# Optimization experiments

Hardware: AMD Instinct MI355X
Metric: run time of the kernel (lower is better)

## Reference

```python
import jax, jax.numpy as jnp
import numpy as np

N = 4096          # vocab / support size (Nini == Nfin)
NBB = 64          # number of topics (columns of b)
NUM_ITER_MAX = 30
STOP_THR = 1e-9


def setup_inputs() -> dict:
    key = jax.random.key(0)
    k1, k2, k3, k4 = jax.random.split(key, 4)
    a = jax.random.uniform(k1, (N, 1), dtype=jnp.float32)
    a = a / jnp.sum(a)                       # source distribution
    b = jax.random.uniform(k2, (N, NBB), dtype=jnp.float32)
    b = b / jnp.sum(b, axis=0, keepdims=True)  # each column a distribution
    lbd = jax.random.uniform(k3, (NBB, 1), dtype=jnp.float32)
    lbd = lbd / jnp.sum(lbd)                 # barycenter weights sum to 1
    M = jax.random.uniform(k4, (N, N), dtype=jnp.float32)  # cost matrix >= 0
    reg = jnp.float32(0.1)
    return {"a": a, "M": M, "b": b, "lbd": lbd, "reg": reg}


def reference(a, M, b, lbd, reg):
    C = jnp.exp(-M / reg)                    # expjit
    lbdT = lbd.T                             # (1, nbb)
    u0 = jnp.ones_like(b)                    # (N, nbb)
    v0 = jnp.ones_like(b)                    # (N, nbb)
    yhat0 = jnp.zeros_like(a)                # (N, 1)

    def cond(state):
        cpt, err, broke, u, v, yhat = state
        return (err > STOP_THR) & (cpt < NUM_ITER_MAX) & (~broke)

    def body(state):
        cpt, err, broke, u, v, yhat = state
        Cu = C @ u                                        # (N, nbb)
        v_new = C.T @ (b / Cu)                            # (N, nbb)
        yhat_new = jnp.prod(v_new ** lbdT, axis=1, keepdims=True)  # (N, 1)
        u_new = yhat_new / v_new                          # (N, nbb)
        bad = (jnp.any(Cu == 0)
               | ~jnp.all(jnp.isfinite(u_new))
               | ~jnp.all(jnp.isfinite(v_new))
               | ~jnp.all(jnp.isfinite(yhat_new)))
        # convergence check every 10 iterations (torch: cpt % 10 == 0)
        lhs = jnp.sum((u_new - u) ** 2) / jnp.sum(u_new ** 2)
        rhs = jnp.sum((v_new - v) ** 2) / jnp.sum(v_new ** 2)
        err_new = jnp.where((cpt % 10 == 0) & ~bad, lhs + rhs, err)
        # on numerical error: revert to previous iterates and break
        u2 = jnp.where(bad, u, u_new)
        v2 = jnp.where(bad, v, v_new)
        yhat2 = jnp.where(bad, yhat, yhat_new)
        cpt2 = cpt + jnp.where(bad, 0, 1)
        return (cpt2, err_new, bad, u2, v2, yhat2)

    state0 = (jnp.int32(0), jnp.float32(1.0), jnp.bool_(False), u0, v0, yhat0)
    *_, yhat = jax.lax.while_loop(cond, body, state0)
    # torch.norm(yhat - a) ** 2 == squared Frobenius norm
    return jnp.sum((yhat - a) ** 2)
```

## Files before the change

### kernel.cpp

```cpp
#include <hip/hip_runtime.h>


typedef __attribute__((ext_vector_type(8))) short bf16x8;
typedef __attribute__((ext_vector_type(8))) unsigned short u16x8;
typedef __attribute__((ext_vector_type(4))) float f32x4;

constexpr int NV     = 4096;
constexpr int NBB_   = 64;
constexpr int ITERS  = 30;
constexpr int KSPLIT = 16;
constexpr int PART   = NV * NBB_;

__device__ __forceinline__ bool finitef(float x) {
  return __builtin_fabsf(x) <= 3.402823466e38f;
}

__device__ __forceinline__ unsigned short f2bf(float x) {
  unsigned int u = __builtin_bit_cast(unsigned int, x);
  return (unsigned short)((u + 0x7fffu + ((u >> 16) & 1u)) >> 16);
}

__device__ __forceinline__ int aswz(int row, int colblk) {
  return row * 64 + (((colblk) ^ (row & 7) ^ (row >> 3)) << 3);
}

__global__ void k_setup(const float* __restrict__ b, float* __restrict__ u,
                        float* __restrict__ v, unsigned short* __restrict__ uT,
                        float* __restrict__ bT, float* __restrict__ yh,
                        float* __restrict__ S) {
  const int gid = blockIdx.x * blockDim.x + threadIdx.x;
  for (int i = gid; i < NV * NBB_; i += 16384) {
    u[i] = 1.0f; v[i] = 1.0f; uT[i] = 0x3F80;
  }
  for (int i = gid; i < NV * NBB_ / 4; i += 16384) {
    const int col = i >> 10;
    const int r4  = (i & 1023) * 4;
#pragma unroll
    for (int q = 0; q < 4; ++q) bT[col * NV + r4 + q] = b[(r4 + q) * NBB_ + col];
  }
  for (int i = gid; i < NV; i += 16384) yh[i] = 0.0f;
  if (gid == 0) {
    int* Si = (int*)S;
    S[0]  = 1.0f;
    Si[1] = 0;
    Si[2] = 0;
    Si[3] = 1; Si[4] = 0;
    Si[5] = 0; Si[6] = 0;
    Si[7] = 0; Si[8] = 0;
#pragma unroll
    for (int q = 16; q < 48; ++q) Si[q] = 0;
  }
}

__global__ void k_cgen(const float* __restrict__ M, const float* __restrict__ regp,
                       unsigned short* __restrict__ Cb) {
  const float ninv = -1.0f / regp[0];
  const size_t i0 = ((size_t)blockIdx.x * 256 + threadIdx.x) * 16;
#pragma unroll
  for (int q = 0; q < 2; ++q) {
    const float4 m0 = *(const float4*)&M[i0 + q * 8];
    const float4 m1 = *(const float4*)&M[i0 + q * 8 + 4];
    u16x8 o;
    o[0] = f2bf(__expf(m0.x * ninv));
    o[1] = f2bf(__expf(m0.y * ninv));
    o[2] = f2bf(__expf(m0.z * ninv));
    o[3] = f2bf(__expf(m0.w * ninv));
    o[4] = f2bf(__expf(m1.x * ninv));
    o[5] = f2bf(__expf(m1.y * ninv));
    o[6] = f2bf(__expf(m1.z * ninv));
    o[7] = f2bf(__expf(m1.w * ninv));
    *(u16x8*)&Cb[i0 + q * 8] = o;
  }
}

template <bool TRANSA>
__global__ __launch_bounds__(256, 4) void k_gemm_mf(
    const unsigned short* __restrict__ A, const unsigned short* __restrict__ BT,
    float* __restrict__ OutP, const int* __restrict__ act) {
  if (*act == 0) return;
  __shared__ unsigned short as_[64 * 64];
  __shared__ unsigned short bsT[64 * 72];
  const int rt = blockIdx.x >> 4;
  const int ks = blockIdx.x & 15;
  const int r0 = rt * 64;
  const int k0 = ks * 256;
  const int t  = threadIdx.x;
  const int w    = t >> 6;
  const int lane = t & 63;
  const int lr   = lane & 15;
  const int lg   = lane >> 4;
  f32x4 acc[4] = {};
  for (int ck = 0; ck < 4; ++ck) {
    const int kb = k0 + ck * 64;
#pragma unroll
    for (int s = 0; s < 2; ++s) {
      const int l = s * 256 + t;
      const int col = l >> 3, k8 = l & 7;
      *(u16x8*)&bsT[col * 72 + k8 * 8] =
          *(const u16x8*)&BT[(size_t)col * NV + kb + k8 * 8];
    }
    if (!TRANSA) {
#pragma unroll
      for (int s = 0; s < 2; ++s) {
        const int l = s * 256 + t;
        const int row = l >> 3, cb = l & 7;
        *(u16x8*)&as_[aswz(row, cb)] =
            *(const u16x8*)&A[(size_t)(r0 + row) * NV + kb + cb * 8];
      }
    } else {
#pragma unroll
      for (int s = 0; s < 2; ++s) {
        const int l = s * 256 + t;
        const int krow = l >> 3, i8 = l & 7;
        const u16x8 m = *(const u16x8*)&A[(size_t)(kb + krow) * NV + r0 + i8 * 8];
#pragma unroll
        for (int e = 0; e < 8; ++e)
          as_[aswz(i8 * 8 + e, krow >> 3) + (krow & 7)] = m[e];
      }
    }
    __syncthreads();
#pragma unroll
    for (int kk = 0; kk < 64; kk += 32) {
      const bf16x8 af = *(const bf16x8*)&as_[aswz(w * 16 + lr, (kk >> 3) + lg)];
#pragma unroll
      for (int ct = 0; ct < 4; ++ct) {
        const bf16x8 bf = *(const bf16x8*)&bsT[(ct * 16 + lr) * 72 + kk + lg * 8];
        acc[ct] = __builtin_amdgcn_mfma_f32_16x16x32_bf16(af, bf, acc[ct], 0, 0, 0);
      }
    }
    __syncthreads();
  }
#pragma unroll
  for (int ct = 0; ct < 4; ++ct) {
    const int col = ct * 16 + lr;
    *(f32x4*)&OutP[(size_t)ks * PART + (size_t)col * NV + r0 + w * 16 + lg * 4] =
        acc[ct];
  }
}

__global__ void k_div_red(const float* __restrict__ bT, const float* __restrict__ CuP,
                          unsigned short* __restrict__ rT, int* __restrict__ badflag,
                          const int* __restrict__ act) {
  if (*act == 0) return;
  const int idx = blockIdx.x * blockDim.x + threadIdx.x;
  const int col = idx >> 10;
  const int r4  = (idx & 1023) * 4;
  const size_t off = (size_t)col * NV + r4;
  float4 s = make_float4(0.f, 0.f, 0.f, 0.f);
#pragma unroll
  for (int k = 0; k < KSPLIT; ++k) {
    const float4 p = *(const float4*)&CuP[(size_t)k * PART + off];
    s.x += p.x; s.y += p.y; s.z += p.z; s.w += p.w;
  }
  const float4 bb = *(const float4*)&bT[off];
  if (s.x == 0.f || s.y == 0.f || s.z == 0.f || s.w == 0.f) atomicOr(badflag, 1);
  ushort4 rr;
  rr.x = f2bf(bb.x / s.x);
  rr.y = f2bf(bb.y / s.y);
  rr.z = f2bf(bb.z / s.z);
  rr.w = f2bf(bb.w / s.w);
  *(ushort4*)&rT[off] = rr;
}

__global__ __launch_bounds__(256, 4) void k_rowwise_commit(
    const float* __restrict__ VaP, const float* __restrict__ lbd,
    float* __restrict__ u, float* __restrict__ v,
    unsigned short* __restrict__ uT, float* __restrict__ yhat,
    float* __restrict__ yhnew, float* __restrict__ Spart,
    float* __restrict__ S, int it) {
  int* Si = (int*)S;
  const int slot = it & 1;
  if (Si[3 + slot] == 0) {
    if (blockIdx.x == 0 && threadIdx.x == 0) Si[3 + (slot ^ 1)] = 0;
    return;
  }
  const int t   = threadIdx.x;
  const int row = blockIdx.x * 64 + (t >> 2);
  const int sub = t & 3;
  const int cb  = sub * 16;
  float vv[16];
#pragma unroll
  for (int c = 0; c < 16; ++c) {
    float s = 0.f;
#pragma unroll
    for (int k = 0; k < KSPLIT; ++k)
      s += VaP[(size_t)k * PART + (size_t)(cb + c) * NV + row];
    vv[c] = s;
  }
  float tq = 0.f;
#pragma unroll
  for (int c = 0; c < 16; ++c) tq += lbd[cb + c] * __logf(vv[c]);
  tq += __shfl_xor(tq, 1);
  tq += __shfl_xor(tq, 2);
  const float yhv = __expf(tq);
  if (sub == 0) yhnew[row] = yhv;
  float s0 = 0.f, s1 = 0.f, s2 = 0.f, s3 = 0.f;
  bool bad = !finitef(yhv);
#pragma unroll
  for (int c = 0; c < 16; ++c) {
    const int idx = row * NBB_ + cb + c;
    const float un = yhv / vv[c];
    const float uo = u[idx];
    const float vo = v[idx];
    u[idx] = un;
    v[idx] = vv[c];
    uT[(size_t)(cb + c) * NV + row] = f2bf(un);
    const float du = un - uo, dv = vv[c] - vo;
    s0 += du * du; s1 += un * un; s2 += dv * dv; s3 += vv[c] * vv[c];
    bad |= !(finitef(un) && finitef(vv[c]));
  }
  if (bad) atomicOr(&Si[7 + slot], 1);
#pragma unroll
  for (int o = 1; o < 64; o <<= 1) {
    s0 += __shfl_xor(s0, o); s1 += __shfl_xor(s1, o);
    s2 += __shfl_xor(s2, o); s3 += __shfl_xor(s3, o);
  }
  __shared__ float wred[4][4];
  __shared__ int lastflag;
  if ((t & 63) == 0) {
    wred[t >> 6][0] = s0; wred[t >> 6][1] = s1;
    wred[t >> 6][2] = s2; wred[t >> 6][3] = s3;
  }
  __syncthreads();
  if (t < 4)
    Spart[blockIdx.x * 4 + t] =
        wred[0][t] + wred[1][t] + wred[2][t] + wred[3][t];
  if (t == 0) {
    __threadfence();
    lastflag = (atomicAdd(&Si[16 + it], 1) == (int)gridDim.x - 1);
  }
  __syncthreads();
  if (!lastflag) return;
  __threadfence();
  const bool com = ((Si[5 + slot] | Si[7 + slot]) == 0);
  __shared__ float cred[4][4];
  {
    float s = Spart[(t >> 2) * 4 + (t & 3)];
#pragma unroll
    for (int o = 4; o < 64; o <<= 1) s += __shfl_xor(s, o);
    if ((t & 63) < 4) cred[t >> 6][t & 3] = s;
  }
  __syncthreads();
  if (t == 0) {
    if (com) {
      const int cpt = Si[1];
      if (cpt % 10 == 0) {
        const float q0 = cred[0][0] + cred[1][0] + cred[2][0] + cred[3][0];
        const float q1 = cred[0][1] + cred[1][1] + cred[2][1] + cred[3][1];
        const float q2 = cred[0][2] + cred[1][2] + cred[2][2] + cred[3][2];
        const float q3 = cred[0][3] + cred[1][3] + cred[2][3] + cred[3][3];
        S[0] = q0 / q1 + q2 / q3;
      }
      Si[1] = cpt + 1;
    } else {
      Si[2] = 1;
    }
    const int ns = slot ^ 1;
    Si[3 + ns] = (S[0] > 1e-9f && Si[1] < ITERS && Si[2] == 0) ? 1 : 0;
    Si[5 + ns] = 0;
    Si[7 + ns] = 0;
  }
  if (com)
    for (int i = t; i < NV; i += 256) yhat[i] = yhnew[i];
}

__global__ void k_final(const float* __restrict__ yhat, const float* __restrict__ a,
                        float* __restrict__ out) {
  __shared__ float red[4];
  const int t = threadIdx.x;
  float s = 0.0f;
  for (int i = t; i < NV; i += 256) {
    const float d = yhat[i] - a[i];
    s = fmaf(d, d, s);
  }
#pragma unroll
  for (int o = 32; o > 0; o >>= 1) s += __shfl_xor(s, o);
  if ((t & 63) == 0) red[t >> 6] = s;
  __syncthreads();
  if (t == 0) out[0] = red[0] + red[1] + red[2] + red[3];
}

extern "C" void kernel_launch(void* const* d_in, const int* in_sizes, int n_in,
                              void* d_out, int out_size, void* d_ws, size_t ws_size,
                              hipStream_t stream) {
  const float* a   = (const float*)d_in[0];
  const float* M   = (const float*)d_in[1];
  const float* b   = (const float*)d_in[2];
  const float* lbd = (const float*)d_in[3];
  const float* reg = (const float*)d_in[4];
  float* out = (float*)d_out;

  char* wsb = (char*)d_ws;
  size_t off = 0;
  auto alloc = [&](size_t bytes) -> void* {
    void* p = wsb + off;
    off += (bytes + 255) & ~(size_t)255;
    return p;
  };
  float*          part  = (float*)alloc(sizeof(float) * (size_t)KSPLIT * PART);
  unsigned short* Cbf   = (unsigned short*)alloc(2 * (size_t)NV * NV);
  float*          bT    = (float*)alloc(sizeof(float) * (size_t)PART);
  unsigned short* uT    = (unsigned short*)alloc(2 * (size_t)PART);
  unsigned short* rT    = (unsigned short*)alloc(2 * (size_t)PART);
  float*          u     = (float*)alloc(sizeof(float) * (size_t)PART);
  float*          v     = (float*)alloc(sizeof(float) * (size_t)PART);
  float*          yh    = (float*)alloc(sizeof(float) * NV);
  float*          yhn   = (float*)alloc(sizeof(float) * NV);
  float*          S     = (float*)alloc(sizeof(float) * 64);
  float*          Spart = (float*)alloc(sizeof(float) * 64 * 4);
  int* Si = (int*)S;

  k_setup<<<dim3(64), dim3(256), 0, stream>>>(b, u, v, uT, bT, yh, S);
  k_cgen<<<dim3(4096), dim3(256), 0, stream>>>(M, reg, Cbf);

  for (int it = 0; it < ITERS; ++it) {
    const int slot = it & 1;
    const int* act = (const int*)(Si + 3 + slot);
    k_gemm_mf<false><<<dim3(1024), dim3(256), 0, stream>>>(Cbf, uT, part, act);
    k_div_red<<<dim3(256), dim3(256), 0, stream>>>(bT, part, rT, Si + 5 + slot, act);
    k_gemm_mf<true><<<dim3(1024), dim3(256), 0, stream>>>(Cbf, rT, part, act);
    k_rowwise_commit<<<dim3(64), dim3(256), 0, stream>>>(part, lbd, u, v, uT, yh,
                                                         yhn, Spart, S, it);
  }

  k_final<<<dim3(1), dim3(256), 0, stream>>>(yh, a, out);
}
```

Baseline: 1.155 ms.

## Fuse split-K GEMMs with reductions, precompute transposed C, drop partial buffers

```diff
diff --git a/kernel.cpp b/kernel.cpp
--- a/kernel.cpp
+++ b/kernel.cpp
@@ -5,11 +5,9 @@
 typedef __attribute__((ext_vector_type(8))) unsigned short u16x8;
 typedef __attribute__((ext_vector_type(4))) float f32x4;
 
-constexpr int NV     = 4096;
-constexpr int NBB_   = 64;
-constexpr int ITERS  = 30;
-constexpr int KSPLIT = 16;
-constexpr int PART   = NV * NBB_;
+constexpr int NV    = 4096;
+constexpr int NBB_  = 64;
+constexpr int ITERS = 30;
 
 __device__ __forceinline__ bool finitef(float x) {
   return __builtin_fabsf(x) <= 3.402823466e38f;
@@ -20,23 +18,12 @@
   return (unsigned short)((u + 0x7fffu + ((u >> 16) & 1u)) >> 16);
 }
 
-__device__ __forceinline__ int aswz(int row, int colblk) {
-  return row * 64 + (((colblk) ^ (row & 7) ^ (row >> 3)) << 3);
-}
-
-__global__ void k_setup(const float* __restrict__ b, float* __restrict__ u,
-                        float* __restrict__ v, unsigned short* __restrict__ uT,
-                        float* __restrict__ bT, float* __restrict__ yh,
+__global__ void k_setup(float* __restrict__ u, float* __restrict__ v,
+                        unsigned short* __restrict__ uT, float* __restrict__ yh,
                         float* __restrict__ S) {
-  const int gid = blockIdx.x * blockDim.x + threadIdx.x;
+  const int gid = blockIdx.x * 256 + threadIdx.x;
   for (int i = gid; i < NV * NBB_; i += 16384) {
     u[i] = 1.0f; v[i] = 1.0f; uT[i] = 0x3F80;
-  }
-  for (int i = gid; i < NV * NBB_ / 4; i += 16384) {
-    const int col = i >> 10;
-    const int r4  = (i & 1023) * 4;
-#pragma unroll
-    for (int q = 0; q < 4; ++q) bT[col * NV + r4 + q] = b[(r4 + q) * NBB_ + col];
   }
   for (int i = gid; i < NV; i += 16384) yh[i] = 0.0f;
   if (gid == 0) {
@@ -47,211 +34,215 @@
     Si[3] = 1; Si[4] = 0;
     Si[5] = 0; Si[6] = 0;
     Si[7] = 0; Si[8] = 0;
-#pragma unroll
-    for (int q = 16; q < 48; ++q) Si[q] = 0;
+    for (int q = 16; q < 16 + ITERS; ++q) Si[q] = 0;
   }
 }
 
 __global__ void k_cgen(const float* __restrict__ M, const float* __restrict__ regp,
-                       unsigned short* __restrict__ Cb) {
+                       unsigned short* __restrict__ Cb,
+                       unsigned short* __restrict__ CTb) {
+  __shared__ float tile[64][65];
+  const int jb = (blockIdx.x & 63) * 64;
+  const int ib = (blockIdx.x >> 6) * 64;
   const float ninv = -1.0f / regp[0];
-  const size_t i0 = ((size_t)blockIdx.x * 256 + threadIdx.x) * 16;
-#pragma unroll
-  for (int q = 0; q < 2; ++q) {
-    const float4 m0 = *(const float4*)&M[i0 + q * 8];
-    const float4 m1 = *(const float4*)&M[i0 + q * 8 + 4];
-    u16x8 o;
-    o[0] = f2bf(__expf(m0.x * ninv));
-    o[1] = f2bf(__expf(m0.y * ninv));
-    o[2] = f2bf(__expf(m0.z * ninv));
-    o[3] = f2bf(__expf(m0.w * ninv));
-    o[4] = f2bf(__expf(m1.x * ninv));
-    o[5] = f2bf(__expf(m1.y * ninv));
-    o[6] = f2bf(__expf(m1.z * ninv));
-    o[7] = f2bf(__expf(m1.w * ninv));
-    *(u16x8*)&Cb[i0 + q * 8] = o;
-  }
-}
-
-template <bool TRANSA>
-__global__ __launch_bounds__(256, 4) void k_gemm_mf(
-    const unsigned short* __restrict__ A, const unsigned short* __restrict__ BT,
-    float* __restrict__ OutP, const int* __restrict__ act) {
+  const int t = threadIdx.x;
+#pragma unroll
+  for (int s = 0; s < 4; ++s) {
+    const int l = s * 256 + t;
+    const int r = l >> 4, c4 = l & 15;
+    const float4 m4 = *(const float4*)&M[(size_t)(ib + r) * NV + jb + c4 * 4];
+    float4 e4;
+    e4.x = __expf(m4.x * ninv);
+    e4.y = __expf(m4.y * ninv);
+    e4.z = __expf(m4.z * ninv);
+    e4.w = __expf(m4.w * ninv);
+    ushort4 o;
+    o.x = f2bf(e4.x); o.y = f2bf(e4.y); o.z = f2bf(e4.z); o.w = f2bf(e4.w);
+    *(ushort4*)&Cb[(size_t)(ib + r) * NV + jb + c4 * 4] = o;
+    *(float4*)&tile[r][c4 * 4] = e4;
+  }
+  __syncthreads();
+#pragma unroll
+  for (int s = 0; s < 4; ++s) {
+    const int l = s * 256 + t;
+    const int r = l >> 4, c4 = l & 15;
+    ushort4 o;
+    o.x = f2bf(tile[c4 * 4 + 0][r]);
+    o.y = f2bf(tile[c4 * 4 + 1][r]);
+    o.z = f2bf(tile[c4 * 4 + 2][r]);
+    o.w = f2bf(tile[c4 * 4 + 3][r]);
+    *(ushort4*)&CTb[(size_t)(jb + r) * NV + ib + c4 * 4] = o;
+  }
+}
+
+__global__ __launch_bounds__(1024) void k_fwd1(
+    const unsigned short* __restrict__ Cb, const unsigned short* __restrict__ uT,
+    const float* __restrict__ b, unsigned short* __restrict__ rT,
+    int* __restrict__ badflag, const int* __restrict__ act) {
   if (*act == 0) return;
-  __shared__ unsigned short as_[64 * 64];
-  __shared__ unsigned short bsT[64 * 72];
-  const int rt = blockIdx.x >> 4;
-  const int ks = blockIdx.x & 15;
-  const int r0 = rt * 64;
-  const int k0 = ks * 256;
-  const int t  = threadIdx.x;
-  const int w    = t >> 6;
-  const int lane = t & 63;
-  const int lr   = lane & 15;
-  const int lg   = lane >> 4;
-  f32x4 acc[4] = {};
-  for (int ck = 0; ck < 4; ++ck) {
-    const int kb = k0 + ck * 64;
-#pragma unroll
-    for (int s = 0; s < 2; ++s) {
-      const int l = s * 256 + t;
-      const int col = l >> 3, k8 = l & 7;
-      *(u16x8*)&bsT[col * 72 + k8 * 8] =
-          *(const u16x8*)&BT[(size_t)col * NV + kb + k8 * 8];
-    }
-    if (!TRANSA) {
-#pragma unroll
-      for (int s = 0; s < 2; ++s) {
-        const int l = s * 256 + t;
-        const int row = l >> 3, cb = l & 7;
-        *(u16x8*)&as_[aswz(row, cb)] =
-            *(const u16x8*)&A[(size_t)(r0 + row) * NV + kb + cb * 8];
-      }
-    } else {
-#pragma unroll
-      for (int s = 0; s < 2; ++s) {
-        const int l = s * 256 + t;
-        const int krow = l >> 3, i8 = l & 7;
-        const u16x8 m = *(const u16x8*)&A[(size_t)(kb + krow) * NV + r0 + i8 * 8];
-#pragma unroll
-        for (int e = 0; e < 8; ++e)
-          as_[aswz(i8 * 8 + e, krow >> 3) + (krow & 7)] = m[e];
-      }
-    }
-    __syncthreads();
-#pragma unroll
-    for (int kk = 0; kk < 64; kk += 32) {
-      const bf16x8 af = *(const bf16x8*)&as_[aswz(w * 16 + lr, (kk >> 3) + lg)];
-#pragma unroll
-      for (int ct = 0; ct < 4; ++ct) {
-        const bf16x8 bf = *(const bf16x8*)&bsT[(ct * 16 + lr) * 72 + kk + lg * 8];
-        acc[ct] = __builtin_amdgcn_mfma_f32_16x16x32_bf16(af, bf, acc[ct], 0, 0, 0);
-      }
-    }
-    __syncthreads();
-  }
-#pragma unroll
-  for (int ct = 0; ct < 4; ++ct) {
-    const int col = ct * 16 + lr;
-    *(f32x4*)&OutP[(size_t)ks * PART + (size_t)col * NV + r0 + w * 16 + lg * 4] =
-        acc[ct];
-  }
-}
-
-__global__ void k_div_red(const float* __restrict__ bT, const float* __restrict__ CuP,
-                          unsigned short* __restrict__ rT, int* __restrict__ badflag,
-                          const int* __restrict__ act) {
-  if (*act == 0) return;
-  const int idx = blockIdx.x * blockDim.x + threadIdx.x;
-  const int col = idx >> 10;
-  const int r4  = (idx & 1023) * 4;
-  const size_t off = (size_t)col * NV + r4;
-  float4 s = make_float4(0.f, 0.f, 0.f, 0.f);
-#pragma unroll
-  for (int k = 0; k < KSPLIT; ++k) {
-    const float4 p = *(const float4*)&CuP[(size_t)k * PART + off];
-    s.x += p.x; s.y += p.y; s.z += p.z; s.w += p.w;
-  }
-  const float4 bb = *(const float4*)&bT[off];
-  if (s.x == 0.f || s.y == 0.f || s.z == 0.f || s.w == 0.f) atomicOr(badflag, 1);
-  ushort4 rr;
-  rr.x = f2bf(bb.x / s.x);
-  rr.y = f2bf(bb.y / s.y);
-  rr.z = f2bf(bb.z / s.z);
-  rr.w = f2bf(bb.w / s.w);
-  *(ushort4*)&rT[off] = rr;
-}
-
-__global__ __launch_bounds__(256, 4) void k_rowwise_commit(
-    const float* __restrict__ VaP, const float* __restrict__ lbd,
-    float* __restrict__ u, float* __restrict__ v,
-    unsigned short* __restrict__ uT, float* __restrict__ yhat,
-    float* __restrict__ yhnew, float* __restrict__ Spart,
-    float* __restrict__ S, int it) {
+  __shared__ f32x4 red4[16][64];
+  const int R = blockIdx.x * 16;
+  const int t = threadIdx.x, w = t >> 6, lane = t & 63;
+  const int lr = lane & 15, lg = lane >> 4;
+  const int ct = w & 3, ks = w >> 2;
+  const unsigned short* Ap = Cb + (size_t)(R + lr) * NV + ks * 1024 + lg * 8;
+  const unsigned short* Bp = uT + (size_t)(ct * 16 + lr) * NV + ks * 1024 + lg * 8;
+  f32x4 acc = {0.f, 0.f, 0.f, 0.f};
+#pragma unroll 8
+  for (int kk = 0; kk < 1024; kk += 32) {
+    const bf16x8 af = *(const bf16x8*)(Ap + kk);
+    const bf16x8 bf = *(const bf16x8*)(Bp + kk);
+    acc = __builtin_amdgcn_mfma_f32_16x16x32_bf16(af, bf, acc, 0, 0, 0);
+  }
+  red4[w][lane] = acc;
+  __syncthreads();
+  if (w < 4) {
+    f32x4 cu = red4[w][lane];
+    cu += red4[w + 4][lane];
+    cu += red4[w + 8][lane];
+    cu += red4[w + 12][lane];
+    bool bad = false;
+    float rq[4];
+#pragma unroll
+    for (int q = 0; q < 4; ++q) {
+      const float cuq = cu[q];
+      const float bq  = b[(R + lg * 4 + q) * NBB_ + w * 16 + lr];
+      bad |= (cuq == 0.0f);
+      rq[q] = bq / cuq;
+    }
+    ushort4 rr;
+    rr.x = f2bf(rq[0]); rr.y = f2bf(rq[1]); rr.z = f2bf(rq[2]); rr.w = f2bf(rq[3]);
+    *(ushort4*)&rT[(size_t)(w * 16 + lr) * NV + R + lg * 4] = rr;
+    if (bad) atomicOr(badflag, 1);
+  }
+}
+
+__global__ __launch_bounds__(1024) void k_fwd2(
+    const unsigned short* __restrict__ CTb, const unsigned short* __restrict__ rT,
+    const float* __restrict__ lbd, float* __restrict__ u, float* __restrict__ v,
+    unsigned short* __restrict__ uT, float* __restrict__ yh,
+    float* __restrict__ yhn, float* __restrict__ Spart, float* __restrict__ S,
+    int it) {
   int* Si = (int*)S;
   const int slot = it & 1;
   if (Si[3 + slot] == 0) {
     if (blockIdx.x == 0 && threadIdx.x == 0) Si[3 + (slot ^ 1)] = 0;
     return;
   }
-  const int t   = threadIdx.x;
-  const int row = blockIdx.x * 64 + (t >> 2);
-  const int sub = t & 3;
-  const int cb  = sub * 16;
-  float vv[16];
-#pragma unroll
-  for (int c = 0; c < 16; ++c) {
-    float s = 0.f;
-#pragma unroll
-    for (int k = 0; k < KSPLIT; ++k)
-      s += VaP[(size_t)k * PART + (size_t)(cb + c) * NV + row];
-    vv[c] = s;
-  }
-  float tq = 0.f;
-#pragma unroll
-  for (int c = 0; c < 16; ++c) tq += lbd[cb + c] * __logf(vv[c]);
-  tq += __shfl_xor(tq, 1);
-  tq += __shfl_xor(tq, 2);
-  const float yhv = __expf(tq);
-  if (sub == 0) yhnew[row] = yhv;
-  float s0 = 0.f, s1 = 0.f, s2 = 0.f, s3 = 0.f;
-  bool bad = !finitef(yhv);
-#pragma unroll
-  for (int c = 0; c < 16; ++c) {
-    const int idx = row * NBB_ + cb + c;
-    const float un = yhv / vv[c];
-    const float uo = u[idx];
-    const float vo = v[idx];
-    u[idx] = un;
-    v[idx] = vv[c];
-    uT[(size_t)(cb + c) * NV + row] = f2bf(un);
-    const float du = un - uo, dv = vv[c] - vo;
-    s0 += du * du; s1 += un * un; s2 += dv * dv; s3 += vv[c] * vv[c];
-    bad |= !(finitef(un) && finitef(vv[c]));
-  }
-  if (bad) atomicOr(&Si[7 + slot], 1);
-#pragma unroll
-  for (int o = 1; o < 64; o <<= 1) {
-    s0 += __shfl_xor(s0, o); s1 += __shfl_xor(s1, o);
-    s2 += __shfl_xor(s2, o); s3 += __shfl_xor(s3, o);
-  }
+  __shared__ f32x4 red4[16][64];
+  __shared__ float yred[4][16];
+  __shared__ float yhl[16];
   __shared__ float wred[4][4];
-  __shared__ int lastflag;
-  if ((t & 63) == 0) {
-    wred[t >> 6][0] = s0; wred[t >> 6][1] = s1;
-    wred[t >> 6][2] = s2; wred[t >> 6][3] = s3;
-  }
-  __syncthreads();
-  if (t < 4)
-    Spart[blockIdx.x * 4 + t] =
-        wred[0][t] + wred[1][t] + wred[2][t] + wred[3][t];
+  __shared__ float cred[16][4];
+  __shared__ int   flags[2];
+  const int R = blockIdx.x * 16;
+  const int t = threadIdx.x, w = t >> 6, lane = t & 63;
+  const int lr = lane & 15, lg = lane >> 4;
+  const int ct = w & 3, ks = w >> 2;
+  const unsigned short* Ap = CTb + (size_t)(R + lr) * NV + ks * 1024 + lg * 8;
+  const unsigned short* Bp = rT + (size_t)(ct * 16 + lr) * NV + ks * 1024 + lg * 8;
+  f32x4 acc = {0.f, 0.f, 0.f, 0.f};
+#pragma unroll 8
+  for (int kk = 0; kk < 1024; kk += 32) {
+    const bf16x8 af = *(const bf16x8*)(Ap + kk);
+    const bf16x8 bf = *(const bf16x8*)(Bp + kk);
+    acc = __builtin_amdgcn_mfma_f32_16x16x32_bf16(af, bf, acc, 0, 0, 0);
+  }
+  red4[w][lane] = acc;
+  __syncthreads();
+  f32x4 vv = {0.f, 0.f, 0.f, 0.f};
+  if (w < 4) {
+    vv = red4[w][lane];
+    vv += red4[w + 4][lane];
+    vv += red4[w + 8][lane];
+    vv += red4[w + 12][lane];
+    const float lb = lbd[w * 16 + lr];
+    float p[4];
+#pragma unroll
+    for (int q = 0; q < 4; ++q) p[q] = lb * __logf(vv[q]);
+#pragma unroll
+    for (int o = 1; o < 16; o <<= 1) {
+#pragma unroll
+      for (int q = 0; q < 4; ++q) p[q] += __shfl_xor(p[q], o);
+    }
+    if (lr == 0) {
+#pragma unroll
+      for (int q = 0; q < 4; ++q) yred[w][lg * 4 + q] = p[q];
+    }
+  }
+  __syncthreads();
+  if (t < 16) {
+    const float s   = yred[0][t] + yred[1][t] + yred[2][t] + yred[3][t];
+    const float yhv = __expf(s);
+    yhl[t] = yhv;
+    yhn[R + t] = yhv;
+    if (!finitef(yhv)) atomicOr(&Si[7 + slot], 1);
+  }
+  __syncthreads();
+  if (w < 4) {
+    float s0 = 0.f, s1 = 0.f, s2 = 0.f, s3 = 0.f;
+    bool bad = false;
+    float un4[4];
+#pragma unroll
+    for (int q = 0; q < 4; ++q) {
+      const int   row = lg * 4 + q;
+      const float yhv = yhl[row];
+      const float un  = yhv / vv[q];
+      un4[q] = un;
+      const int idx = (R + row) * NBB_ + w * 16 + lr;
+      const float uo = u[idx], vo = v[idx];
+      u[idx] = un;
+      v[idx] = vv[q];
+      const float du = un - uo, dv = vv[q] - vo;
+      s0 += du * du; s1 += un * un; s2 += dv * dv; s3 += vv[q] * vv[q];
+      bad |= !(finitef(un) && finitef(vv[q]));
+    }
+    ushort4 uu;
+    uu.x = f2bf(un4[0]); uu.y = f2bf(un4[1]); uu.z = f2bf(un4[2]); uu.w = f2bf(un4[3]);
+    *(ushort4*)&uT[(size_t)(w * 16 + lr) * NV + R + lg * 4] = uu;
+    if (bad) atomicOr(&Si[7 + slot], 1);
+#pragma unroll
+    for (int o = 1; o < 64; o <<= 1) {
+      s0 += __shfl_xor(s0, o); s1 += __shfl_xor(s1, o);
+      s2 += __shfl_xor(s2, o); s3 += __shfl_xor(s3, o);
+    }
+    if (lane == 0) {
+      wred[w][0] = s0; wred[w][1] = s1; wred[w][2] = s2; wred[w][3] = s3;
+    }
+  }
+  __syncthreads();
   if (t == 0) {
+#pragma unroll
+    for (int c = 0; c < 4; ++c)
+      Spart[blockIdx.x * 4 + c] =
+          wred[0][c] + wred[1][c] + wred[2][c] + wred[3][c];
     __threadfence();
-    lastflag = (atomicAdd(&Si[16 + it], 1) == (int)gridDim.x - 1);
-  }
-  __syncthreads();
-  if (!lastflag) return;
+    flags[0] = (atomicAdd(&Si[16 + it], 1) == (int)gridDim.x - 1);
+  }
+  __syncthreads();
+  if (!flags[0]) return;
   __threadfence();
-  const bool com = ((Si[5 + slot] | Si[7 + slot]) == 0);
-  __shared__ float cred[4][4];
   {
-    float s = Spart[(t >> 2) * 4 + (t & 3)];
+    const int c = t & 3;
+    float s = Spart[(t >> 2) * 4 + c];
 #pragma unroll
     for (int o = 4; o < 64; o <<= 1) s += __shfl_xor(s, o);
-    if ((t & 63) < 4) cred[t >> 6][t & 3] = s;
+    if (lane < 4) cred[w][lane] = s;
   }
   __syncthreads();
   if (t == 0) {
-    if (com) {
+    float q0 = 0.f, q1 = 0.f, q2 = 0.f, q3 = 0.f;
+#pragma unroll
+    for (int i = 0; i < 16; ++i) {
+      q0 += cred[i][0]; q1 += cred[i][1]; q2 += cred[i][2]; q3 += cred[i][3];
+    }
+    const bool bad = (Si[5 + slot] | Si[7 + slot]) != 0;
+    int com = 0;
+    if (!bad) {
       const int cpt = Si[1];
-      if (cpt % 10 == 0) {
-        const float q0 = cred[0][0] + cred[1][0] + cred[2][0] + cred[3][0];
-        const float q1 = cred[0][1] + cred[1][1] + cred[2][1] + cred[3][1];
-        const float q2 = cred[0][2] + cred[1][2] + cred[2][2] + cred[3][2];
-        const float q3 = cred[0][3] + cred[1][3] + cred[2][3] + cred[3][3];
-        S[0] = q0 / q1 + q2 / q3;
-      }
+      if (cpt % 10 == 0) S[0] = q0 / q1 + q2 / q3;
       Si[1] = cpt + 1;
+      com = 1;
     } else {
       Si[2] = 1;
     }
@@ -259,9 +250,11 @@
     Si[3 + ns] = (S[0] > 1e-9f && Si[1] < ITERS && Si[2] == 0) ? 1 : 0;
     Si[5 + ns] = 0;
     Si[7 + ns] = 0;
-  }
-  if (com)
-    for (int i = t; i < NV; i += 256) yhat[i] = yhnew[i];
+    flags[1] = com;
+  }
+  __syncthreads();
+  if (flags[1])
+    for (int i = t; i < NV; i += 1024) yh[i] = yhn[i];
 }
 
 __global__ void k_final(const float* __restrict__ yhat, const float* __restrict__ a,
@@ -297,30 +290,27 @@
     off += (bytes + 255) & ~(size_t)255;
     return p;
   };
-  float*          part  = (float*)alloc(sizeof(float) * (size_t)KSPLIT * PART);
   unsigned short* Cbf   = (unsigned short*)alloc(2 * (size_t)NV * NV);
-  float*          bT    = (float*)alloc(sizeof(float) * (size_t)PART);
-  unsigned short* uT    = (unsigned short*)alloc(2 * (size_t)PART);
-  unsigned short* rT    = (unsigned short*)alloc(2 * (size_t)PART);
-  float*          u     = (float*)alloc(sizeof(float) * (size_t)PART);
-  float*          v     = (float*)alloc(sizeof(float) * (size_t)PART);
+  unsigned short* CTbf  = (unsigned short*)alloc(2 * (size_t)NV * NV);
+  unsigned short* uT    = (unsigned short*)alloc(2 * (size_t)NV * NBB_);
+  unsigned short* rT    = (unsigned short*)alloc(2 * (size_t)NV * NBB_);
+  float*          u     = (float*)alloc(sizeof(float) * (size_t)NV * NBB_);
+  float*          v     = (float*)alloc(sizeof(float) * (size_t)NV * NBB_);
   float*          yh    = (float*)alloc(sizeof(float) * NV);
   float*          yhn   = (float*)alloc(sizeof(float) * NV);
   float*          S     = (float*)alloc(sizeof(float) * 64);
-  float*          Spart = (float*)alloc(sizeof(float) * 64 * 4);
+  float*          Spart = (float*)alloc(sizeof(float) * 256 * 4);
   int* Si = (int*)S;
 
-  k_setup<<<dim3(64), dim3(256), 0, stream>>>(b, u, v, uT, bT, yh, S);
-  k_cgen<<<dim3(4096), dim3(256), 0, stream>>>(M, reg, Cbf);
+  k_setup<<<dim3(64), dim3(256), 0, stream>>>(u, v, uT, yh, S);
+  k_cgen<<<dim3(4096), dim3(256), 0, stream>>>(M, reg, Cbf, CTbf);
 
   for (int it = 0; it < ITERS; ++it) {
     const int slot = it & 1;
     const int* act = (const int*)(Si + 3 + slot);
-    k_gemm_mf<false><<<dim3(1024), dim3(256), 0, stream>>>(Cbf, uT, part, act);
-    k_div_red<<<dim3(256), dim3(256), 0, stream>>>(bT, part, rT, Si + 5 + slot, act);
-    k_gemm_mf<true><<<dim3(1024), dim3(256), 0, stream>>>(Cbf, rT, part, act);
-    k_rowwise_commit<<<dim3(64), dim3(256), 0, stream>>>(part, lbd, u, v, uT, yh,
-                                                         yhn, Spart, S, it);
+    k_fwd1<<<dim3(256), dim3(1024), 0, stream>>>(Cbf, uT, b, rT, Si + 5 + slot, act);
+    k_fwd2<<<dim3(256), dim3(1024), 0, stream>>>(CTbf, rT, lbd, u, v, uT, yh,
+                                                 yhn, Spart, S, it);
   }
 
   k_final<<<dim3(1), dim3(256), 0, stream>>>(yh, a, out);
```

Measured after the change: 1.684 ms. 45.8% more time.
